# Kernel tuning notes

Measured on AMD Instinct MI355X. Metric: run time of the kernel, lower is better.

Reference implementation:

```python
import jax, jax.numpy as jnp
import numpy as np

B, N, D, O, L = 16, 2000, 128, 64, 3  # batch, n_nodes, hidden_dim, output_dim, n_layers


def _init(key, shape, fan_in):
    return jax.random.normal(key, shape, jnp.float32) / np.sqrt(fan_in).astype(np.float32)


def setup_inputs() -> dict:
    key = jax.random.key(0)
    ks = jax.random.split(key, 8)
    return {
        "coords": jax.random.normal(ks[0], (B, N, 2), jnp.float32),
        "enc_w0": _init(ks[1], (2, D), 2),
        "enc_b0": jnp.zeros((D,), jnp.float32),
        "enc_w1": _init(ks[2], (D, D), D),
        "enc_b1": jnp.zeros((D,), jnp.float32),
        "gat_W": _init(ks[3], (L, D, D), D),      # per-layer GAT projection (no bias)
        "gat_a1": _init(ks[4], (L, D), 2 * D),    # first half of attention vector a
        "gat_a2": _init(ks[5], (L, D), 2 * D),    # second half of attention vector a
        "proj_w": _init(ks[6], (D, O), D),
        "proj_b": jnp.zeros((O,), jnp.float32),
    }


def _leaky(x):
    return jnp.where(x >= 0, x, 0.2 * x)  # LeakyReLU(0.2)


def reference(coords, enc_w0, enc_b0, enc_w1, enc_b1, gat_W, gat_a1, gat_a2, proj_w, proj_b):
    # node encoder: Linear -> ReLU -> Linear
    h = jax.nn.relu(coords @ enc_w0 + enc_b0) @ enc_w1 + enc_b1  # [B,N,D]
    n_layers = gat_W.shape[0]
    for l in range(n_layers):
        Wh = h @ gat_W[l]                      # [B,N,D]
        # additive GAT attention: e_ij = leakyrelu(a1.Wh_i + a2.Wh_j)
        # (equivalent to a([Wh_i || Wh_j]) without materializing N*N*2D tensor)
        e1 = Wh @ gat_a1[l]                    # [B,N]
        e2 = Wh @ gat_a2[l]                    # [B,N]
        e = _leaky(e1[:, :, None] + e2[:, None, :])  # [B,N,N]
        # adj is all-ones in forward() so the masked_fill is a no-op
        att = jax.nn.softmax(e, axis=-1)       # [B,N,N]; dropout is identity (eval)
        h = jax.nn.relu(att @ Wh)              # [B,N,D]
    return h @ proj_w + proj_b                 # [B,N,O]
```

## Files before the change

### kernel.cpp

```cpp
#include <hip/hip_runtime.h>
#include <hip/hip_bf16.h>

using bf16 = __hip_bfloat16;

#define BATCH 16
#define NNODE 2000
#define DIM   128
#define ODIM  64
#define NLAYER 3
#define BN    (BATCH*NNODE)
#define NCH   500
#define CKS2  4
#define SFX   502
#define NSEG  25
#define SEGC  20

#define OFF_COORDS 0
#define OFF_EW0    64000
#define OFF_EB0    64256
#define OFF_EW1    64384
#define OFF_EB1    80768
#define OFF_GW     80896
#define OFF_GA1    130048
#define OFF_GA2    130432
#define OFF_PW     130816
#define OFF_PB     139008
#define CVT_TOT    139072

#define PK_GAT(l)  (32768 + (l)*32768)
#define PK_PROJ    131072
#define PK_TOT     147456

typedef __attribute__((ext_vector_type(8))) short bf16x8;
typedef __attribute__((ext_vector_type(4))) float f32x4;

__device__ __forceinline__ unsigned short f2bf(float f){
    union { float f; unsigned u; } x; x.f = f;
    unsigned r = (x.u + 0x7FFFu + ((x.u >> 16) & 1u)) >> 16;
    return (unsigned short)r;
}
__device__ __forceinline__ float bf2f(unsigned short h){
    union { unsigned u; float f; } x; x.u = ((unsigned)h) << 16;
    return x.f;
}
__device__ __forceinline__ unsigned ordu(float f){
    union { float f; unsigned u; } x; x.f = f;
    return (x.u & 0x80000000u) ? ~x.u : (x.u | 0x80000000u);
}
__device__ __forceinline__ float iordu(unsigned u){
    union { unsigned u; float f; } x;
    x.u = (u & 0x80000000u) ? (u ^ 0x80000000u) : ~u;
    return x.f;
}

struct InPtrs { const void* p[10]; };

__global__ void convert_all_k(InPtrs in, float* __restrict__ dst, float* __restrict__ flag)
{
    __shared__ int scnt[256];
    const unsigned short* raw = (const unsigned short*)in.p[0];
    int t = threadIdx.x, c = 0;
    for (int k = t; k < 2048; k += 256){
        unsigned short u = raw[2*k];
        int e = (u >> 7) & 0xFF;
        if (e >= 100 && e <= 140) ++c;
    }
    scnt[t] = c;
    __syncthreads();
    for (int s = 128; s; s >>= 1){ if (t < s) scnt[t] += scnt[t+s]; __syncthreads(); }
    const bool isbf16 = (scnt[0] >= 1800);
    if (blockIdx.x == 0 && t == 0) flag[0] = isbf16 ? 1.0f : 0.0f;

    const int off[11] = {OFF_COORDS,OFF_EW0,OFF_EB0,OFF_EW1,OFF_EB1,
                         OFF_GW,OFF_GA1,OFF_GA2,OFF_PW,OFF_PB,CVT_TOT};
    int i = blockIdx.x*256 + t;
    if (i >= CVT_TOT) return;
    int seg = 0;
    #pragma unroll
    for (int s = 1; s < 10; ++s) if (i >= off[s]) seg = s;
    int li = i - off[seg];
    if (isbf16) dst[i] = __bfloat162float(((const bf16*)in.p[seg])[li]);
    else        dst[i] = ((const float*)in.p[seg])[li];
}

__global__ __launch_bounds__(256) void prep_k(const float* __restrict__ cvt,
                                              unsigned short* __restrict__ pk,
                                              float* __restrict__ wa)
{
    const int mi = blockIdx.x, t = threadIdx.x;
    if (mi < 3){
        const float* W; unsigned short* dst; int N;
        if (mi == 0)      { W = cvt + OFF_GW + 1*DIM*DIM;  dst = pk + PK_GAT(1); N = 128; }
        else if (mi == 1) { W = cvt + OFF_GW + 2*DIM*DIM;  dst = pk + PK_GAT(2); N = 128; }
        else              { W = cvt + OFF_PW;              dst = pk + PK_PROJ;   N = 64;  }
        const int tot = 128*N;
        unsigned short* dh = dst;
        unsigned short* dl = dst + tot;
        for (int e = t; e < tot; e += 256){
            int col = e >> 7, k = e & 127;
            float v = W[k*N + col];
            unsigned short hb = f2bf(v);
            unsigned short lb = f2bf(v - bf2f(hb));
            dh[e] = hb;
            dl[e] = lb;
        }
    } else {
        for (int idx = t; idx < 3*256; idx += 256){
            const int l = idx >> 8, rem = idx & 255, half = rem >> 7, r = rem & 127;
            const float* W  = cvt + OFF_GW + l*DIM*DIM;
            const float* av = cvt + (half ? OFF_GA2 : OFF_GA1) + l*DIM;
            float s = 0.f;
            for (int c2 = 0; c2 < 128; ++c2) s = fmaf(W[r*128 + c2], av[c2], s);
            wa[l*256 + half*128 + r] = s;
        }
    }
}

__global__ __launch_bounds__(128) void prep2_k(const float* __restrict__ cvt,
    unsigned short* __restrict__ pk, const float* __restrict__ wa,
    float* __restrict__ u12, float* __restrict__ bfuse, float* __restrict__ su)
{
    const int b = blockIdx.x, t = threadIdx.x;
    const float* w1 = cvt + OFF_EW1;
    const float* W0 = cvt + OFF_GW;
    if (b < 128){
        float acc = 0.f;
        for (int d = 0; d < 128; ++d) acc = fmaf(w1[b*DIM + d], W0[d*DIM + t], acc);
        unsigned short hb = f2bf(acc), lb = f2bf(acc - bf2f(hb));
        unsigned short* dst = pk + PK_GAT(0);
        dst[t*128 + b]         = hb;
        dst[16384 + t*128 + b] = lb;
    } else if (b == 128){
        const float* b1 = cvt + OFF_EB1;
        float acc = 0.f;
        for (int d = 0; d < 128; ++d) acc = fmaf(b1[d], W0[d*DIM + t], acc);
        bfuse[t] = acc;
        if (t < 2){
            float s = 0.f;
            for (int d = 0; d < 128; ++d) s = fmaf(b1[d], wa[t*128 + d], s);
            su[t] = s;
        }
    } else {
        float a1 = 0.f, a2 = 0.f;
        for (int d = 0; d < 128; ++d){
            float w = w1[t*DIM + d];
            a1 = fmaf(w, wa[d],       a1);
            a2 = fmaf(w, wa[128 + d], a2);
        }
        u12[t]       = a1;
        u12[128 + t] = a2;
    }
}


__global__ __launch_bounds__(256) void gat0mfma_k(const float* __restrict__ cvt,
    const unsigned short* __restrict__ pk, const float* __restrict__ u12,
    const float* __restrict__ su, const float* __restrict__ bfuse,
    float* __restrict__ Wh, float* __restrict__ e1p, float* __restrict__ e2p)
{
    __shared__ unsigned short sAh[64*128], sAl[64*128];
    const int t = threadIdx.x, r0 = blockIdx.x*64;
    const int wv = t >> 6, l = t & 63, lc = l & 15, lk = l >> 4;
    const unsigned short* ph = pk;
    const unsigned short* pl = pk + 16384;
    bf16x8 bh[2][4], bl[2][4];
    #pragma unroll
    for (int cg = 0; cg < 2; ++cg){
        const int col = wv*32 + cg*16 + lc;
        #pragma unroll
        for (int kc = 0; kc < 4; ++kc){
            const int k0 = kc*32 + lk*8;
            bh[cg][kc] = *(const bf16x8*)&ph[col*128 + k0];
            bl[cg][kc] = *(const bf16x8*)&pl[col*128 + k0];
        }
    }
    const int row = t >> 2, g = t & 3;
    const float* coords = cvt + OFF_COORDS;
    const float* w0  = cvt + OFF_EW0;
    const float* b0v = cvt + OFF_EB0;
    const int node = r0 + row;
    const float c0 = coords[2*node], c1 = coords[2*node+1];
    char* shb = (char*)sAh; char* slb = (char*)sAl;
    const int swz = (row & 7) << 4;
    float e1 = 0.f, e2 = 0.f;
    #pragma unroll
    for (int i = 0; i < 8; ++i){
        const int ch = g + i*4, k0 = ch*4;
        float4 wa0 = *(const float4*)&w0[k0];
        float4 wb0 = *(const float4*)&w0[DIM + k0];
        float4 bq  = *(const float4*)&b0v[k0];
        float4 v;
        v.x = fmaf(c0, wa0.x, fmaf(c1, wb0.x, bq.x)); v.x = v.x > 0.f ? v.x : 0.f;
        v.y = fmaf(c0, wa0.y, fmaf(c1, wb0.y, bq.y)); v.y = v.y > 0.f ? v.y : 0.f;
        v.z = fmaf(c0, wa0.z, fmaf(c1, wb0.z, bq.z)); v.z = v.z > 0.f ? v.z : 0.f;
        v.w = fmaf(c0, wa0.w, fmaf(c1, wb0.w, bq.w)); v.w = v.w > 0.f ? v.w : 0.f;
        float4 q1 = *(const float4*)&u12[k0];
        float4 q2 = *(const float4*)&u12[128 + k0];
        e1 = fmaf(v.x,q1.x, fmaf(v.y,q1.y, fmaf(v.z,q1.z, fmaf(v.w,q1.w, e1))));
        e2 = fmaf(v.x,q2.x, fmaf(v.y,q2.y, fmaf(v.z,q2.z, fmaf(v.w,q2.w, e2))));
        ushort4 hq, lq;
        hq.x = f2bf(v.x); lq.x = f2bf(v.x - bf2f(hq.x));
        hq.y = f2bf(v.y); lq.y = f2bf(v.y - bf2f(hq.y));
        hq.z = f2bf(v.z); lq.z = f2bf(v.z - bf2f(hq.z));
        hq.w = f2bf(v.w); lq.w = f2bf(v.w - bf2f(hq.w));
        const int bo = (ch*8) ^ swz;
        *(ushort4*)(shb + row*256 + bo) = hq;
        *(ushort4*)(slb + row*256 + bo) = lq;
    }
    e1 += __shfl_xor(e1, 1); e1 += __shfl_xor(e1, 2);
    e2 += __shfl_xor(e2, 1); e2 += __shfl_xor(e2, 2);
    if (g == 0){ e1p[r0 + row] = e1 + su[0]; e2p[r0 + row] = e2 + su[1]; }
    __syncthreads();
    f32x4 acc[4][2] = {};
    #pragma unroll
    for (int m = 0; m < 4; ++m){
        const int ar = m*16 + lc, asw = (ar & 7) << 4;
        #pragma unroll
        for (int kc = 0; kc < 4; ++kc){
            const int bo = (kc*64 + lk*16) ^ asw;
            bf16x8 ah = *(bf16x8*)(shb + ar*256 + bo);
            bf16x8 al = *(bf16x8*)(slb + ar*256 + bo);
            #pragma unroll
            for (int cg = 0; cg < 2; ++cg){
                acc[m][cg] = __builtin_amdgcn_mfma_f32_16x16x32_bf16(ah, bh[cg][kc], acc[m][cg], 0, 0, 0);
                acc[m][cg] = __builtin_amdgcn_mfma_f32_16x16x32_bf16(ah, bl[cg][kc], acc[m][cg], 0, 0, 0);
                acc[m][cg] = __builtin_amdgcn_mfma_f32_16x16x32_bf16(al, bh[cg][kc], acc[m][cg], 0, 0, 0);
            }
        }
    }
    #pragma unroll
    for (int m = 0; m < 4; ++m){
        const int rg = r0 + m*16 + lk*4;
        #pragma unroll
        for (int cg = 0; cg < 2; ++cg){
            const int col = wv*32 + cg*16 + lc;
            const float bb = bfuse[col];
            #pragma unroll
            for (int j = 0; j < 4; ++j) Wh[(size_t)(rg+j)*DIM + col] = acc[m][cg][j] + bb;
        }
    }
}

__global__ __launch_bounds__(256) void gatmfma_k(const float* __restrict__ A,
    const unsigned short* __restrict__ pk, const float* __restrict__ wa,
    float* __restrict__ Wh, float* __restrict__ e1p, float* __restrict__ e2p)
{
    __shared__ unsigned short sAh[64*128], sAl[64*128];
    const int t = threadIdx.x, r0 = blockIdx.x*64;
    const int wv = t >> 6, l = t & 63, lc = l & 15, lk = l >> 4;
    const unsigned short* ph = pk;
    const unsigned short* pl = pk + 16384;
    bf16x8 bh[2][4], bl[2][4];
    #pragma unroll
    for (int cg = 0; cg < 2; ++cg){
        const int col = wv*32 + cg*16 + lc;
        #pragma unroll
        for (int kc = 0; kc < 4; ++kc){
            const int k0 = kc*32 + lk*8;
            bh[cg][kc] = *(const bf16x8*)&ph[col*128 + k0];
            bl[cg][kc] = *(const bf16x8*)&pl[col*128 + k0];
        }
    }
    const int row = t >> 2, g = t & 3;
    const float* Ar = A + (size_t)(r0 + row)*DIM;
    char* shb = (char*)sAh; char* slb = (char*)sAl;
    const int swz = (row & 7) << 4;
    float e1 = 0.f, e2 = 0.f;
    #pragma unroll
    for (int i = 0; i < 8; ++i){
        const int ch = g + i*4;
        float4 a  = *(const float4*)&Ar[ch*4];
        float4 u1 = *(const float4*)&wa[ch*4];
        float4 u2 = *(const float4*)&wa[128 + ch*4];
        e1 = fmaf(a.x,u1.x, fmaf(a.y,u1.y, fmaf(a.z,u1.z, fmaf(a.w,u1.w, e1))));
        e2 = fmaf(a.x,u2.x, fmaf(a.y,u2.y, fmaf(a.z,u2.z, fmaf(a.w,u2.w, e2))));
        ushort4 hq, lq;
        hq.x = f2bf(a.x); lq.x = f2bf(a.x - bf2f(hq.x));
        hq.y = f2bf(a.y); lq.y = f2bf(a.y - bf2f(hq.y));
        hq.z = f2bf(a.z); lq.z = f2bf(a.z - bf2f(hq.z));
        hq.w = f2bf(a.w); lq.w = f2bf(a.w - bf2f(hq.w));
        const int bo = (ch*8) ^ swz;
        *(ushort4*)(shb + row*256 + bo) = hq;
        *(ushort4*)(slb + row*256 + bo) = lq;
    }
    e1 += __shfl_xor(e1, 1); e1 += __shfl_xor(e1, 2);
    e2 += __shfl_xor(e2, 1); e2 += __shfl_xor(e2, 2);
    if (g == 0){ e1p[r0 + row] = e1; e2p[r0 + row] = e2; }
    __syncthreads();
    f32x4 acc[4][2] = {};
    #pragma unroll
    for (int m = 0; m < 4; ++m){
        const int ar = m*16 + lc, asw = (ar & 7) << 4;
        #pragma unroll
        for (int kc = 0; kc < 4; ++kc){
            const int bo = (kc*64 + lk*16) ^ asw;
            bf16x8 ah = *(bf16x8*)(shb + ar*256 + bo);
            bf16x8 al = *(bf16x8*)(slb + ar*256 + bo);
            #pragma unroll
            for (int cg = 0; cg < 2; ++cg){
                acc[m][cg] = __builtin_amdgcn_mfma_f32_16x16x32_bf16(ah, bh[cg][kc], acc[m][cg], 0, 0, 0);
                acc[m][cg] = __builtin_amdgcn_mfma_f32_16x16x32_bf16(ah, bl[cg][kc], acc[m][cg], 0, 0, 0);
                acc[m][cg] = __builtin_amdgcn_mfma_f32_16x16x32_bf16(al, bh[cg][kc], acc[m][cg], 0, 0, 0);
            }
        }
    }
    #pragma unroll
    for (int m = 0; m < 4; ++m){
        const int rg = r0 + m*16 + lk*4;
        #pragma unroll
        for (int cg = 0; cg < 2; ++cg){
            const int col = wv*32 + cg*16 + lc;
            #pragma unroll
            for (int j = 0; j < 4; ++j) Wh[(size_t)(rg+j)*DIM + col] = acc[m][cg][j];
        }
    }
}

__global__ __launch_bounds__(256) void projmfma_k(const float* __restrict__ A,
    const unsigned short* __restrict__ pk, const float* __restrict__ bias,
    void* __restrict__ outp, const float* __restrict__ flag)
{
    __shared__ unsigned short sAh[64*128], sAl[64*128];
    const int t = threadIdx.x, r0 = blockIdx.x*64;
    const int wv = t >> 6, l = t & 63, lc = l & 15, lk = l >> 4;
    const unsigned short* ph = pk;
    const unsigned short* pl = pk + 8192;
    bf16x8 bh[4], bl[4];
    const int col = wv*16 + lc;
    #pragma unroll
    for (int kc = 0; kc < 4; ++kc){
        const int k0 = kc*32 + lk*8;
        bh[kc] = *(const bf16x8*)&ph[col*128 + k0];
        bl[kc] = *(const bf16x8*)&pl[col*128 + k0];
    }
    const int row = t >> 2, g = t & 3;
    const float* Ar = A + (size_t)(r0 + row)*DIM;
    char* shb = (char*)sAh; char* slb = (char*)sAl;
    const int swz = (row & 7) << 4;
    #pragma unroll
    for (int i = 0; i < 8; ++i){
        const int ch = g + i*4;
        float4 a = *(const float4*)&Ar[ch*4];
        ushort4 hq, lq;
        hq.x = f2bf(a.x); lq.x = f2bf(a.x - bf2f(hq.x));
        hq.y = f2bf(a.y); lq.y = f2bf(a.y - bf2f(hq.y));
        hq.z = f2bf(a.z); lq.z = f2bf(a.z - bf2f(hq.z));
        hq.w = f2bf(a.w); lq.w = f2bf(a.w - bf2f(hq.w));
        const int bo = (ch*8) ^ swz;
        *(ushort4*)(shb + row*256 + bo) = hq;
        *(ushort4*)(slb + row*256 + bo) = lq;
    }
    __syncthreads();
    f32x4 acc[4] = {};
    #pragma unroll
    for (int m = 0; m < 4; ++m){
        const int ar = m*16 + lc, asw = (ar & 7) << 4;
        #pragma unroll
        for (int kc = 0; kc < 4; ++kc){
            const int bo = (kc*64 + lk*16) ^ asw;
            bf16x8 ah = *(bf16x8*)(shb + ar*256 + bo);
            bf16x8 al = *(bf16x8*)(slb + ar*256 + bo);
            acc[m] = __builtin_amdgcn_mfma_f32_16x16x32_bf16(ah, bh[kc], acc[m], 0, 0, 0);
            acc[m] = __builtin_amdgcn_mfma_f32_16x16x32_bf16(ah, bl[kc], acc[m], 0, 0, 0);
            acc[m] = __builtin_amdgcn_mfma_f32_16x16x32_bf16(al, bh[kc], acc[m], 0, 0, 0);
        }
    }
    const float bb = bias[col];
    const bool isbf = (flag[0] != 0.0f);
    #pragma unroll
    for (int m = 0; m < 4; ++m){
        const int rg = r0 + m*16 + lk*4;
        #pragma unroll
        for (int j = 0; j < 4; ++j){
            float v = acc[m][j] + bb;
            size_t p = (size_t)(rg+j)*ODIM + col;
            if (isbf) ((bf16*)outp)[p] = __float2bfloat16(v);
            else      ((float*)outp)[p] = v;
        }
    }
}

#define WAVE_FENCE() __asm__ volatile("" ::: "memory")
__global__ void sortF_k(const float* __restrict__ e2p, const float* __restrict__ e1p,
    int* __restrict__ sidx, float* __restrict__ wp, float* __restrict__ wn,
    float* __restrict__ sps, float* __restrict__ sns, int* __restrict__ loArr)
{
    __shared__ unsigned long long kv[2048];
    const int b = blockIdx.x, t = threadIdx.x;
    for (int i = t; i < 2048; i += 1024)
        kv[i] = (i < NNODE) ? (((unsigned long long)ordu(e2p[b*NNODE + i]) << 32) | (unsigned)i)
                            : 0xFFFFFFFFFFFFFFFFull;
    __syncthreads();

    #pragma unroll 1
    for (int size = 2; size <= 128; size <<= 1){
        #pragma unroll 1
        for (int stride = size >> 1; stride > 0; stride >>= 1){
            int i = 2*t - (t & (stride-1));
            int j = i + stride;
            bool asc = ((i & size) == 0);
            unsigned long long ki = kv[i], kj = kv[j];
            bool sw = asc ? (ki > kj) : (ki < kj);
            if (sw){ kv[i] = kj; kv[j] = ki; }
            WAVE_FENCE();
        }
    }
    __syncthreads();

    #pragma unroll 1
    for (int size = 256; size <= 2048; size <<= 1){
        #pragma unroll 1
        for (int stride = size >> 1; stride >= 128; stride >>= 1){
            int i = 2*t - (t & (stride-1));
            int j = i + stride;
            bool asc = ((i & size) == 0);
            unsigned long long ki = kv[i], kj = kv[j];
            bool sw = asc ? (ki > kj) : (ki < kj);
            if (sw){ kv[i] = kj; kv[j] = ki; }
            __syncthreads();
        }
        #pragma unroll 1
        for (int stride = 64; stride > 0; stride >>= 1){
            int i = 2*t - (t & (stride-1));
            int j = i + stride;
            bool asc = ((i & size) == 0);
            unsigned long long ki = kv[i], kj = kv[j];
            bool sw = asc ? (ki > kj) : (ki < kj);
            if (sw){ kv[i] = kj; kv[j] = ki; }
            WAVE_FENCE();
        }
        __syncthreads();
    }

    const float mx = iordu((unsigned)(kv[NNODE-1] >> 32));
    for (int i = t; i < NNODE; i += 1024){
        unsigned long long key = kv[i];
        float val = iordu((unsigned)(key >> 32));
        sidx[b*NNODE+i] = (int)(key & 0xFFFFFFFFull);
        wp  [b*NNODE+i] = __expf(val - mx);
        wn  [b*NNODE+i] = __expf(0.2f*(val - mx));
    }
    #pragma unroll
    for (int q = 0; q < 2; ++q){
        const int i = t + q*1024;
        if (i < NNODE){
            float e1v = e1p[b*NNODE + i];
            float s = e1v + mx;
            float m = (s >= 0.f) ? s : 0.2f*s;
            sps[b*NNODE + i] = __expf(s - m);
            sns[b*NNODE + i] = __expf(0.2f*s - m);
            unsigned tt = ordu(-e1v);
            int lo = 0, hi = NNODE;
            while (lo < hi){
                int mid = (lo + hi) >> 1;
                if ((unsigned)(kv[mid] >> 32) < tt) lo = mid + 1; else hi = mid;
            }
            loArr[b*NNODE + i] = lo;
        }
    }
}

__global__ __launch_bounds__(128) void chunkSums_k(const float* __restrict__ Wh,
    const int* __restrict__ sidx, const float* __restrict__ wp, const float* __restrict__ wn,
    float* __restrict__ chunkP, float* __restrict__ chunkN,
    float* __restrict__ schunkP, float* __restrict__ schunkN)
{
    const int b = blockIdx.x / NCH, c = blockIdx.x % NCH, d = threadIdx.x;
    const int base = b*NNODE;
    float sp=0.f, sn=0.f, ssp=0.f, ssn=0.f;
    #pragma unroll
    for (int r = c*CKS2; r < c*CKS2 + CKS2; ++r){
        int j = sidx[base + r];
        float whv = Wh[((size_t)base + j)*DIM + d];
        float wpv = wp[base + r], wnv = wn[base + r];
        sp = fmaf(wpv, whv, sp);  sn = fmaf(wnv, whv, sn);
        ssp += wpv;  ssn += wnv;
    }
    const int idx = b*NCH + c;
    chunkP[(size_t)idx*DIM + d] = sp;
    chunkN[(size_t)idx*DIM + d] = sn;
    if (d == 0){ schunkP[idx] = ssp; schunkN[idx] = ssn; }
}

__global__ __launch_bounds__(128) void segTot_k(
    const float* __restrict__ chunkP, const float* __restrict__ chunkN,
    const float* __restrict__ schunkP, const float* __restrict__ schunkN,
    float* __restrict__ segP, float* __restrict__ segN,
    float* __restrict__ ssegP, float* __restrict__ ssegN)
{
    const int b = blockIdx.x / NSEG, seg = blockIdx.x % NSEG, d = threadIdx.x;
    const int c0 = seg*SEGC;
    float aP = 0.f, aN = 0.f;
    #pragma unroll
    for (int k = 0; k < SEGC; ++k){
        aP += chunkP[((size_t)b*NCH + c0 + k)*DIM + d];
        aN += chunkN[((size_t)b*NCH + c0 + k)*DIM + d];
    }
    segP[((size_t)b*NSEG + seg)*DIM + d] = aP;
    segN[((size_t)b*NSEG + seg)*DIM + d] = aN;
    if (d == 0){
        float sP = 0.f, sN = 0.f;
        #pragma unroll
        for (int k = 0; k < SEGC; ++k){
            sP += schunkP[b*NCH + c0 + k];
            sN += schunkN[b*NCH + c0 + k];
        }
        ssegP[b*NSEG + seg] = sP;
        ssegN[b*NSEG + seg] = sN;
    }
}

__global__ __launch_bounds__(128) void sfxFill_k(
    const float* __restrict__ chunkP, const float* __restrict__ chunkN,
    const float* __restrict__ schunkP, const float* __restrict__ schunkN,
    const float* __restrict__ segP, const float* __restrict__ segN,
    const float* __restrict__ ssegP, const float* __restrict__ ssegN,
    float* __restrict__ sfxP, float* __restrict__ sfxN,
    float* __restrict__ sfxSP, float* __restrict__ sfxSN)
{
    const int b = blockIdx.x / NSEG, seg = blockIdx.x % NSEG, d = threadIdx.x;
    const size_t sb = (size_t)b*SFX;
    float aP = 0.f, aN = 0.f;
    for (int s = seg + 1; s < NSEG; ++s){
        aP += segP[((size_t)b*NSEG + s)*DIM + d];
        aN += segN[((size_t)b*NSEG + s)*DIM + d];
    }
    const int c0 = seg*SEGC;
    #pragma unroll
    for (int k = SEGC-1; k >= 0; --k){
        aP += chunkP[((size_t)b*NCH + c0 + k)*DIM + d];
        aN += chunkN[((size_t)b*NCH + c0 + k)*DIM + d];
        sfxP[(sb + c0 + k)*DIM + d] = aP;
        sfxN[(sb + c0 + k)*DIM + d] = aN;
    }
    if (seg == NSEG-1){
        sfxP[(sb + NCH    )*DIM + d] = 0.f;
        sfxP[(sb + NCH + 1)*DIM + d] = 0.f;
        sfxN[(sb + NCH    )*DIM + d] = 0.f;
        sfxN[(sb + NCH + 1)*DIM + d] = 0.f;
    }
    if (d == 0){
        float sP = 0.f, sN = 0.f;
        for (int s = seg + 1; s < NSEG; ++s){
            sP += ssegP[b*NSEG + s];
            sN += ssegN[b*NSEG + s];
        }
        #pragma unroll
        for (int k = SEGC-1; k >= 0; --k){
            sP += schunkP[b*NCH + c0 + k];
            sN += schunkN[b*NCH + c0 + k];
            sfxSP[b*SFX + c0 + k] = sP;
            sfxSN[b*SFX + c0 + k] = sN;
        }
        if (seg == NSEG-1){
            sfxSP[b*SFX + NCH] = 0.f;  sfxSP[b*SFX + NCH + 1] = 0.f;
            sfxSN[b*SFX + NCH] = 0.f;  sfxSN[b*SFX + NCH + 1] = 0.f;
        }
    }
}

__global__ __launch_bounds__(128) void out4_k(const float* __restrict__ Wh,
    const int* __restrict__ sidx, const float* __restrict__ wp, const float* __restrict__ wn,
    const float* __restrict__ sfxP, const float* __restrict__ sfxN,
    const float* __restrict__ sfxSP, const float* __restrict__ sfxSN,
    const float* __restrict__ sps, const float* __restrict__ sns,
    const int* __restrict__ loArr, float* __restrict__ h)
{
    __shared__ int   slo[16];
    __shared__ float ssp[16], ssn[16];
    const int b = blockIdx.x / 125, g16 = blockIdx.x % 125, d = threadIdx.x;
    const int base = b*NNODE, row0 = g16*16;

    if (d < 16){
        int row = base + row0 + d;
        slo[d] = loArr[row];
        ssp[d] = sps[row];
        ssn[d] = sns[row];
    }
    __syncthreads();

    const size_t sb = (size_t)b*SFX;
    const float totN  = sfxN[sb*DIM + d];
    const float totSN = sfxSN[b*SFX];

    #pragma unroll 4
    for (int k = 0; k < 16; ++k){
        const int lo = slo[k];
        const int cl = lo >> 2;
        float suffP = sfxP[(sb + cl + 1)*DIM + d];
        float suffN = sfxN[(sb + cl + 1)*DIM + d];
        float sSP   = sfxSP[b*SFX + cl + 1];
        float sSN   = sfxSN[b*SFX + cl + 1];
        int rend = (cl + 1)*CKS2; if (rend > NNODE) rend = NNODE;
        #pragma unroll 1
        for (int r = lo; r < rend; ++r){
            int j = sidx[base + r];
            float whv = Wh[((size_t)base + j)*DIM + d];
            float wpv = wp[base + r], wnv = wn[base + r];
            suffP = fmaf(wpv, whv, suffP);
            suffN = fmaf(wnv, whv, suffN);
            sSP += wpv;  sSN += wnv;
        }
        const float spsv = ssp[k], snsv = ssn[k];
        float numer = spsv*suffP + snsv*(totN - suffN);
        float Z     = spsv*sSP   + snsv*(totSN - sSN);
        float v = numer / Z;
        h[((size_t)base + row0 + k)*DIM + d] = (v > 0.f) ? v : ((v == v) ? 0.f : v);
    }
}

extern "C" void kernel_launch(void* const* d_in, const int* in_sizes, int n_in,
                              void* d_out, int out_size, void* d_ws, size_t ws_size,
                              hipStream_t stream)
{
    (void)in_sizes; (void)n_in; (void)out_size; (void)ws_size;

    float* f = (float*)d_ws;
    float* flag    = f;  f += 4;
    float* cvt     = f;  f += CVT_TOT;
    float* h       = f;  f += (size_t)BN*DIM;
    float* Wh      = f;  f += (size_t)BN*DIM;
    float* chunkP  = f;  f += (size_t)BATCH*NCH*DIM;
    float* chunkN  = f;  f += (size_t)BATCH*NCH*DIM;
    float* sfxP    = f;  f += (size_t)BATCH*SFX*DIM;
    float* sfxN    = f;  f += (size_t)BATCH*SFX*DIM;
    float* segP    = f;  f += (size_t)BATCH*NSEG*DIM;
    float* segN    = f;  f += (size_t)BATCH*NSEG*DIM;
    float* schunkP = f;  f += BATCH*NCH;
    float* schunkN = f;  f += BATCH*NCH;
    float* sfxSP   = f;  f += BATCH*SFX;
    float* sfxSN   = f;  f += BATCH*SFX;
    float* ssegP   = f;  f += BATCH*NSEG;
    float* ssegN   = f;  f += BATCH*NSEG;
    float* e1p     = f;  f += BN;
    float* e2p     = f;  f += BN;
    float* wp      = f;  f += BN;
    float* wn      = f;  f += BN;
    float* sps     = f;  f += BN;
    float* sns     = f;  f += BN;
    int*   sidx    = (int*)f;  f += BN;
    int*   loArr   = (int*)f;  f += BN;
    unsigned short* pk = (unsigned short*)f;
    float* wa      = (float*)(pk + PK_TOT);
    float* u12     = wa + 768;
    float* bfuse   = u12 + 256;
    float* su      = bfuse + 128;

    InPtrs ip;
    for (int i = 0; i < 10; ++i) ip.p[i] = d_in[i];
    convert_all_k<<<(CVT_TOT+255)/256, 256, 0, stream>>>(ip, cvt, flag);

    prep_k<<<4, 256, 0, stream>>>(cvt, pk, wa);
    prep2_k<<<130, 128, 0, stream>>>(cvt, pk, wa, u12, bfuse, su);

    for (int l = 0; l < NLAYER; ++l){
        if (l == 0)
            gat0mfma_k<<<BN/64, 256, 0, stream>>>(cvt, pk + PK_GAT(0), u12, su, bfuse,
                                                  Wh, e1p, e2p);
        else
            gatmfma_k<<<BN/64, 256, 0, stream>>>(h, pk + PK_GAT(l), wa + l*256, Wh, e1p, e2p);
        sortF_k<<<BATCH, 1024, 0, stream>>>(e2p, e1p, sidx, wp, wn, sps, sns, loArr);
        chunkSums_k<<<BATCH*NCH, DIM, 0, stream>>>(Wh, sidx, wp, wn,
                                                   chunkP, chunkN, schunkP, schunkN);
        segTot_k<<<BATCH*NSEG, 128, 0, stream>>>(chunkP, chunkN, schunkP, schunkN,
                                                 segP, segN, ssegP, ssegN);
        sfxFill_k<<<BATCH*NSEG, 128, 0, stream>>>(chunkP, chunkN, schunkP, schunkN,
                                                  segP, segN, ssegP, ssegN,
                                                  sfxP, sfxN, sfxSP, sfxSN);
        out4_k<<<BATCH*125, DIM, 0, stream>>>(Wh, sidx, wp, wn, sfxP, sfxN, sfxSP, sfxSN,
                                              sps, sns, loArr, h);
    }

    projmfma_k<<<BN/64, 256, 0, stream>>>(h, pk + PK_PROJ, cvt + OFF_PB, d_out, flag);
}
```

Measured before the change: 294.0 us.

## Split per-batch bitonic sort into segment sorts plus merge-by-rank kernel

Replaces the single 1024-thread-per-batch bitonic sort with two kernels. The first sorts eight 256-key segments per batch in parallel blocks. The second loads all sorted segments and computes each key's global rank by binary searching the other segments, then scatters indices and weights. The loArr lookup also becomes a sum of per-segment binary searches. This spreads the work over many more blocks than the 16 used before, at the cost of an extra launch and a global round trip for the keys.

New measurement: 296.6 us. About the same (+0.9%).

```diff
diff --git a/kernel.cpp b/kernel.cpp
--- a/kernel.cpp
+++ b/kernel.cpp
@@ -14,6 +14,7 @@
 #define SFX   502
 #define NSEG  25
 #define SEGC  20
+#define PADKEY 0xFFFFFFFFFFFFFFFFull
 
 #define OFF_COORDS 0
 #define OFF_EW0    64000
@@ -381,17 +382,20 @@
 }
 
 #define WAVE_FENCE() __asm__ volatile("" ::: "memory")
-__global__ void sortF_k(const float* __restrict__ e2p, const float* __restrict__ e1p,
-    int* __restrict__ sidx, float* __restrict__ wp, float* __restrict__ wn,
-    float* __restrict__ sps, float* __restrict__ sns, int* __restrict__ loArr)
-{
-    __shared__ unsigned long long kv[2048];
-    const int b = blockIdx.x, t = threadIdx.x;
-    for (int i = t; i < 2048; i += 1024)
-        kv[i] = (i < NNODE) ? (((unsigned long long)ordu(e2p[b*NNODE + i]) << 32) | (unsigned)i)
-                            : 0xFFFFFFFFFFFFFFFFull;
-    __syncthreads();
-
+__global__ __launch_bounds__(128) void sortA_k(const float* __restrict__ e2p,
+                                               unsigned long long* __restrict__ skeys)
+{
+    __shared__ unsigned long long kv[256];
+    const int b = blockIdx.x >> 3, s = blockIdx.x & 7, t = threadIdx.x;
+    const int base = b*NNODE, g0 = s*256;
+    #pragma unroll
+    for (int q = 0; q < 2; ++q){
+        int i = t + q*128;
+        int gi = g0 + i;
+        kv[i] = (gi < NNODE) ? (((unsigned long long)ordu(e2p[base+gi]) << 32) | (unsigned)gi)
+                             : PADKEY;
+    }
+    __syncthreads();
     #pragma unroll 1
     for (int size = 2; size <= 128; size <<= 1){
         #pragma unroll 1
@@ -406,57 +410,85 @@
         }
     }
     __syncthreads();
-
+    {
+        unsigned long long ki = kv[t], kj = kv[t + 128];
+        if (ki > kj){ kv[t] = kj; kv[t + 128] = ki; }
+        __syncthreads();
+    }
     #pragma unroll 1
-    for (int size = 256; size <= 2048; size <<= 1){
+    for (int stride = 64; stride > 0; stride >>= 1){
+        int i = 2*t - (t & (stride-1));
+        int j = i + stride;
+        unsigned long long ki = kv[i], kj = kv[j];
+        if (ki > kj){ kv[i] = kj; kv[j] = ki; }
+        WAVE_FENCE();
+    }
+    __syncthreads();
+    #pragma unroll
+    for (int q = 0; q < 2; ++q){
+        int i = t + q*128;
+        skeys[(size_t)b*2048 + g0 + i] = kv[i];
+    }
+}
+
+__global__ __launch_bounds__(256) void sortB_k(const unsigned long long* __restrict__ skeys,
+    const float* __restrict__ e1p, int* __restrict__ sidx, float* __restrict__ wp,
+    float* __restrict__ wn, float* __restrict__ sps, float* __restrict__ sns,
+    int* __restrict__ loArr)
+{
+    __shared__ __align__(16) unsigned long long kv[2048];
+    __shared__ float smax[4];
+    const int b = blockIdx.x >> 3, s = blockIdx.x & 7, t = threadIdx.x;
+    const int base = b*NNODE;
+    float pm = -3.0e38f;
+    #pragma unroll
+    for (int q = 0; q < 8; ++q){
+        int i = t + q*256;
+        unsigned long long k = skeys[(size_t)b*2048 + i];
+        kv[i] = k;
+        if (k != PADKEY) pm = fmaxf(pm, iordu((unsigned)(k >> 32)));
+    }
+    #pragma unroll
+    for (int m = 32; m; m >>= 1) pm = fmaxf(pm, __shfl_xor(pm, m));
+    if ((t & 63) == 0) smax[t >> 6] = pm;
+    __syncthreads();
+    const float mx = fmaxf(fmaxf(smax[0], smax[1]), fmaxf(smax[2], smax[3]));
+
+    {
+        unsigned long long k = kv[s*256 + t];
+        if (k != PADKEY){
+            int rank = t;
+            #pragma unroll 1
+            for (int s2 = 0; s2 < 8; ++s2){
+                if (s2 == s) continue;
+                const int o = s2*256;
+                int lo2 = 0, hi2 = 256;
+                while (lo2 < hi2){ int mid = (lo2+hi2)>>1; if (kv[o+mid] < k) lo2 = mid+1; else hi2 = mid; }
+                rank += lo2;
+            }
+            float val = iordu((unsigned)(k >> 32));
+            sidx[base + rank] = (int)(k & 0xFFFFFFFFull);
+            wp  [base + rank] = __expf(val - mx);
+            wn  [base + rank] = __expf(0.2f*(val - mx));
+        }
+    }
+    if (t < 250){
+        const int i = s*250 + t;
+        float e1v = e1p[base + i];
+        float sv = e1v + mx;
+        float m = (sv >= 0.f) ? sv : 0.2f*sv;
+        sps[base + i] = __expf(sv - m);
+        sns[base + i] = __expf(0.2f*sv - m);
+        const unsigned long long tk = ((unsigned long long)ordu(-e1v)) << 32;
+        int lo = 0;
         #pragma unroll 1
-        for (int stride = size >> 1; stride >= 128; stride >>= 1){
-            int i = 2*t - (t & (stride-1));
-            int j = i + stride;
-            bool asc = ((i & size) == 0);
-            unsigned long long ki = kv[i], kj = kv[j];
-            bool sw = asc ? (ki > kj) : (ki < kj);
-            if (sw){ kv[i] = kj; kv[j] = ki; }
-            __syncthreads();
-        }
-        #pragma unroll 1
-        for (int stride = 64; stride > 0; stride >>= 1){
-            int i = 2*t - (t & (stride-1));
-            int j = i + stride;
-            bool asc = ((i & size) == 0);
-            unsigned long long ki = kv[i], kj = kv[j];
-            bool sw = asc ? (ki > kj) : (ki < kj);
-            if (sw){ kv[i] = kj; kv[j] = ki; }
-            WAVE_FENCE();
-        }
-        __syncthreads();
-    }
-
-    const float mx = iordu((unsigned)(kv[NNODE-1] >> 32));
-    for (int i = t; i < NNODE; i += 1024){
-        unsigned long long key = kv[i];
-        float val = iordu((unsigned)(key >> 32));
-        sidx[b*NNODE+i] = (int)(key & 0xFFFFFFFFull);
-        wp  [b*NNODE+i] = __expf(val - mx);
-        wn  [b*NNODE+i] = __expf(0.2f*(val - mx));
-    }
-    #pragma unroll
-    for (int q = 0; q < 2; ++q){
-        const int i = t + q*1024;
-        if (i < NNODE){
-            float e1v = e1p[b*NNODE + i];
-            float s = e1v + mx;
-            float m = (s >= 0.f) ? s : 0.2f*s;
-            sps[b*NNODE + i] = __expf(s - m);
-            sns[b*NNODE + i] = __expf(0.2f*s - m);
-            unsigned tt = ordu(-e1v);
-            int lo = 0, hi = NNODE;
-            while (lo < hi){
-                int mid = (lo + hi) >> 1;
-                if ((unsigned)(kv[mid] >> 32) < tt) lo = mid + 1; else hi = mid;
-            }
-            loArr[b*NNODE + i] = lo;
-        }
+        for (int s2 = 0; s2 < 8; ++s2){
+            const int o = s2*256;
+            int lo2 = 0, hi2 = 256;
+            while (lo2 < hi2){ int mid = (lo2+hi2)>>1; if (kv[o+mid] < tk) lo2 = mid+1; else hi2 = mid; }
+            lo += lo2;
+        }
+        loArr[base + i] = lo;
     }
 }
 
@@ -640,6 +672,7 @@
     float* sns     = f;  f += BN;
     int*   sidx    = (int*)f;  f += BN;
     int*   loArr   = (int*)f;  f += BN;
+    unsigned long long* skeys = (unsigned long long*)f;  f += BATCH*2048*2;
     unsigned short* pk = (unsigned short*)f;
     float* wa      = (float*)(pk + PK_TOT);
     float* u12     = wa + 768;
@@ -659,7 +692,8 @@
                                                   Wh, e1p, e2p);
         else
             gatmfma_k<<<BN/64, 256, 0, stream>>>(h, pk + PK_GAT(l), wa + l*256, Wh, e1p, e2p);
-        sortF_k<<<BATCH, 1024, 0, stream>>>(e2p, e1p, sidx, wp, wn, sps, sns, loArr);
+        sortA_k<<<BATCH*8, 128, 0, stream>>>(e2p, skeys);
+        sortB_k<<<BATCH*8, 256, 0, stream>>>(skeys, e1p, sidx, wp, wn, sps, sns, loArr);
         chunkSums_k<<<BATCH*NCH, DIM, 0, stream>>>(Wh, sidx, wp, wn,
                                                    chunkP, chunkN, schunkP, schunkN);
         segTot_k<<<BATCH*NSEG, 128, 0, stream>>>(chunkP, chunkN, schunkP, schunkN,
```
